# Kernel optimization log

Hardware: AMD Instinct MI355X
Metric: run time of the kernel (lower is better)

The kernel has to match this reference:

```python
import jax, jax.numpy as jnp
import numpy as np

G = 56          # voxel grid resolution per axis
N = 65536
K = 27          # 3x3x3 kernel offsets
C_IN = 128
C_OUT = 128


def _build_rulebook():
    """Submanifold conv rulebook: for each kernel offset, (input_row, output_row) pairs.

    Padded to P=N pairs per offset; invalid pairs use in_idx=0 and out_idx=N
    (a dummy output slot that is dropped), so shapes are static.
    """
    rng = np.random.default_rng(0)
    keys = np.sort(rng.choice(G ** 3, size=N, replace=False)).astype(np.int64)
    x = keys // (G * G)
    y = (keys // G) % G
    z = keys % G
    in_idx = np.zeros((K, N), dtype=np.int32)
    out_idx = np.full((K, N), N, dtype=np.int32)
    k = 0
    for dx in (-1, 0, 1):
        for dy in (-1, 0, 1):
            for dz in (-1, 0, 1):
                nx, ny, nz = x + dx, y + dy, z + dz
                valid = (nx >= 0) & (nx < G) & (ny >= 0) & (ny < G) & (nz >= 0) & (nz < G)
                nkey = (nx * G + ny) * G + nz
                pos = np.searchsorted(keys, np.clip(nkey, 0, G ** 3 - 1))
                pos = np.clip(pos, 0, N - 1)
                found = valid & (keys[pos] == nkey)
                cnt = int(found.sum())
                in_idx[k, :cnt] = pos[found]
                out_idx[k, :cnt] = np.nonzero(found)[0]
                k += 1
    return jnp.asarray(in_idx), jnp.asarray(out_idx)


def setup_inputs() -> dict:
    key = jax.random.key(0)
    k1, k2, k3 = jax.random.split(key, 3)
    fan_in = K * C_IN
    features = jax.random.normal(k1, (N, C_IN), dtype=jnp.float32)
    weight = jax.random.normal(k2, (K, C_IN, C_OUT), dtype=jnp.float32) * (1.0 / np.sqrt(fan_in))
    bias = jax.random.normal(k3, (C_OUT,), dtype=jnp.float32) * 0.01
    in_idx, out_idx = _build_rulebook()
    return {"features": features, "weight": weight, "bias": bias,
            "in_idx": in_idx, "out_idx": out_idx}


def reference(features, weight, bias, in_idx, out_idx):
    # gather: [K, P, C_in]
    gathered = features[in_idx]
    # per-offset GEMM: [K, P, C_out]
    contrib = jnp.einsum('kpc,kcd->kpd', gathered, weight)
    n = features.shape[0]
    c_out = weight.shape[-1]
    # scatter-accumulate into N real rows + 1 dummy row for padded pairs
    out = jnp.zeros((n + 1, c_out), dtype=features.dtype)
    out = out.at[out_idx.reshape(-1)].add(contrib.reshape(-1, c_out))
    return out[:n] + bias
```

## Files before the change

kernel.cpp:

```cpp
#include <hip/hip_runtime.h>
#include <hip/hip_bf16.h>
#include <stdint.h>

#define NV   65536
#define KOFF 27
#define CIN  128
#define COUT 128

typedef __bf16 bf16x8 __attribute__((ext_vector_type(8)));
typedef float  f32x4  __attribute__((ext_vector_type(4)));

__device__ __forceinline__ void async_copy16(void* lds, const void* g) {
    __builtin_amdgcn_global_load_lds(
        (const __attribute__((address_space(1))) void*)g,
        (__attribute__((address_space(3))) void*)lds,
        16, 0, 0);
}

#define JOB_A_BLOCKS 4097
#define JOB_B_BLOCKS 1728
#define JOB_C_BLOCKS 6912

__global__ void k_prep_all(const float* __restrict__ f,
                           uint4* __restrict__ fb4,
                           const float* __restrict__ w,
                           __hip_bfloat16* __restrict__ wt,
                           const int* __restrict__ in_idx,
                           const int* __restrict__ out_idx,
                           int* __restrict__ nbr) {
    const int b = blockIdx.x;
    const int t = threadIdx.x;
    if (b < JOB_A_BLOCKS) {
        int i = b * 256 + t;
        int total8  = (NV + 1) * CIN / 8;
        int nvalid8 = NV * CIN / 8;
        if (i >= total8) return;
        union { uint4 u; __hip_bfloat16 h[8]; } p;
        if (i < nvalid8) {
            const float4* f4 = (const float4*)f;
            float4 a = f4[i * 2];
            float4 c = f4[i * 2 + 1];
            p.h[0] = __float2bfloat16(a.x);
            p.h[1] = __float2bfloat16(a.y);
            p.h[2] = __float2bfloat16(a.z);
            p.h[3] = __float2bfloat16(a.w);
            p.h[4] = __float2bfloat16(c.x);
            p.h[5] = __float2bfloat16(c.y);
            p.h[6] = __float2bfloat16(c.z);
            p.h[7] = __float2bfloat16(c.w);
        } else {
            p.u = make_uint4(0, 0, 0, 0);
        }
        fb4[i] = p.u;
    } else if (b < JOB_A_BLOCKS + JOB_B_BLOCKS) {
        int i = (b - JOB_A_BLOCKS) * 256 + t;
        int k    = i >> 14;
        int cin  = (i >> 7) & 127;
        int cout = i & 127;
        wt[k * 16384 + cout * 128 + cin] = __float2bfloat16(w[i]);
    } else {
        int i = (b - JOB_A_BLOCKS - JOB_B_BLOCKS) * 256 + t;
        int k = i >> 16;
        int p = i & (NV - 1);
        const int* ok = out_idx + k * NV;
        int cur  = ok[p];
        int prev = (p == 0) ? -1 : ok[p - 1];
        int* nb = nbr + k * NV;
        if (cur < NV) nb[cur] = in_idx[k * NV + p];
        for (int j = prev + 1; j < cur && j < NV; ++j) nb[j] = -1;
    }
}

__global__ __launch_bounds__(256, 2)
void sp_conv_main(const __hip_bfloat16* __restrict__ feats,
                  const __hip_bfloat16* __restrict__ wt,
                  const int* __restrict__ nbr,
                  const float* __restrict__ bias,
                  float* __restrict__ out) {
    __shared__ unsigned char smem[65536];
    unsigned char* smA = smem;
    unsigned char* smB = smem + 32768;

    const int t   = threadIdx.x;
    const int bid = blockIdx.x;
    const int tile0 = ((bid & 7) * 64 + (bid >> 3)) * 128;

    const int w    = t >> 6;
    const int lane = t & 63;
    const int lr   = lane & 15;
    const int quad = lane >> 4;
    const int m0   = (w >> 1) * 64;
    const int n0   = (w & 1) * 64;

    const int srow   = t >> 4;
    const int sbyte  = ((t & 15) ^ srow) * 16;

    f32x4 acc[4][4] = {};

    const unsigned char* featsB = (const unsigned char*)feats;
    const unsigned char* wtB    = (const unsigned char*)wt;

    int arows[8];
    {
        const int* nbr0 = nbr + tile0;
        #pragma unroll
        for (int i = 0; i < 8; ++i) arows[i] = nbr0[i * 16 + srow];
    }

    for (int k = 0; k < KOFF; ++k) {
        const unsigned char* wk = wtB + (size_t)k * 32768;
        #pragma unroll
        for (int i = 0; i < 8; ++i) {
            unsigned ar = min((unsigned)arows[i], (unsigned)NV);
            async_copy16(smA + i * 4096 + t * 16,
                         featsB + (size_t)ar * 256 + sbyte);
            async_copy16(smB + i * 4096 + t * 16,
                         wk + (i * 16 + srow) * 256 + sbyte);
        }
        __syncthreads();

        if (k + 1 < KOFF) {
            const int* nbrn = nbr + (k + 1) * NV + tile0;
            #pragma unroll
            for (int i = 0; i < 8; ++i) arows[i] = nbrn[i * 16 + srow];
        }

        #pragma unroll
        for (int ks = 0; ks < 4; ++ks) {
            bf16x8 af[4], bfr[4];
            #pragma unroll
            for (int mt = 0; mt < 4; ++mt) {
                int row = m0 + mt * 16 + lr;
                int pch = ((ks * 4 + quad) ^ lr) * 16;
                af[mt] = *(const bf16x8*)(smA + row * 256 + pch);
            }
            #pragma unroll
            for (int nt = 0; nt < 4; ++nt) {
                int row = n0 + nt * 16 + lr;
                int pch = ((ks * 4 + quad) ^ lr) * 16;
                bfr[nt] = *(const bf16x8*)(smB + row * 256 + pch);
            }
            #pragma unroll
            for (int mt = 0; mt < 4; ++mt)
                #pragma unroll
                for (int nt = 0; nt < 4; ++nt)
                    acc[mt][nt] = __builtin_amdgcn_mfma_f32_16x16x32_bf16(
                        af[mt], bfr[nt], acc[mt][nt], 0, 0, 0);
        }
        __syncthreads();
    }

    float bv[4];
    #pragma unroll
    for (int nt = 0; nt < 4; ++nt) bv[nt] = bias[n0 + nt * 16 + lr];

    #pragma unroll
    for (int mt = 0; mt < 4; ++mt) {
        #pragma unroll
        for (int nt = 0; nt < 4; ++nt) {
            #pragma unroll
            for (int r = 0; r < 4; ++r) {
                int grow = tile0 + m0 + mt * 16 + quad * 4 + r;
                out[(size_t)grow * COUT + n0 + nt * 16 + lr] =
                    acc[mt][nt][r] + bv[nt];
            }
        }
    }
}


extern "C" void kernel_launch(void* const* d_in, const int* in_sizes, int n_in,
                              void* d_out, int out_size, void* d_ws, size_t ws_size,
                              hipStream_t stream) {
    const float* features = (const float*)d_in[0];
    const float* weight   = (const float*)d_in[1];
    const float* bias     = (const float*)d_in[2];
    const int*   in_idx   = (const int*)d_in[3];
    const int*   out_idx  = (const int*)d_in[4];
    float* out = (float*)d_out;

    uint8_t* ws = (uint8_t*)d_ws;
    size_t off = 0;
    __hip_bfloat16* feats_bf = (__hip_bfloat16*)(ws + off);
    off += (size_t)(NV + 1) * CIN * 2;
    off = (off + 255) & ~(size_t)255;
    __hip_bfloat16* wt_bf = (__hip_bfloat16*)(ws + off);
    off += (size_t)KOFF * CIN * COUT * 2;
    off = (off + 255) & ~(size_t)255;
    int* nbr = (int*)(ws + off);

    k_prep_all<<<JOB_A_BLOCKS + JOB_B_BLOCKS + JOB_C_BLOCKS, 256, 0, stream>>>(
        features, (uint4*)feats_bf, weight, wt_bf, in_idx, out_idx, nbr);

    sp_conv_main<<<NV / 128, 256, 0, stream>>>(feats_bf, wt_bf, nbr, bias, out);
}
```

Baseline: 180.2 us.

## Use 32x32 MFMA tiles, LDS-transpose weights, and memset-based neighbor table scatter

The main GEMM loop moves from 16x16x32 MFMA on a 4x4 grid of tiles to 32x32x16 MFMA on a 2x2 grid, which cuts LDS fragment reads per wave and the number of MFMA issues. The weight transpose now stages 64x64 tiles through shared memory so both global reads and writes are coalesced. The neighbor table is built by a memset to -1 followed by a vectorized int4 scatter into an (NV+1)-stride table, so padded pairs land in a dummy slot and the gap-filling loop goes away. This adds an extra memset launch and a larger neighbor table.

```diff
diff --git a/kernel.cpp b/kernel.cpp
--- a/kernel.cpp
+++ b/kernel.cpp
@@ -8,7 +8,7 @@
 #define COUT 128
 
 typedef __bf16 bf16x8 __attribute__((ext_vector_type(8)));
-typedef float  f32x4  __attribute__((ext_vector_type(4)));
+typedef float  f32x16 __attribute__((ext_vector_type(16)));
 
 __device__ __forceinline__ void async_copy16(void* lds, const void* g) {
     __builtin_amdgcn_global_load_lds(
@@ -18,16 +18,17 @@
 }
 
 #define JOB_A_BLOCKS 4097
-#define JOB_B_BLOCKS 1728
-#define JOB_C_BLOCKS 6912
+#define JOB_B_BLOCKS 108
+#define JOB_S_BLOCKS 1728
 
 __global__ void k_prep_all(const float* __restrict__ f,
                            uint4* __restrict__ fb4,
                            const float* __restrict__ w,
                            __hip_bfloat16* __restrict__ wt,
-                           const int* __restrict__ in_idx,
-                           const int* __restrict__ out_idx,
+                           const int4* __restrict__ in4,
+                           const int4* __restrict__ out4,
                            int* __restrict__ nbr) {
+    __shared__ float tb[64][65];
     const int b = blockIdx.x;
     const int t = threadIdx.x;
     if (b < JOB_A_BLOCKS) {
@@ -53,21 +54,35 @@
         }
         fb4[i] = p.u;
     } else if (b < JOB_A_BLOCKS + JOB_B_BLOCKS) {
-        int i = (b - JOB_A_BLOCKS) * 256 + t;
-        int k    = i >> 14;
-        int cin  = (i >> 7) & 127;
-        int cout = i & 127;
-        wt[k * 16384 + cout * 128 + cin] = __float2bfloat16(w[i]);
+        int bb = b - JOB_A_BLOCKS;
+        int k    = bb >> 2;
+        int r0   = ((bb >> 1) & 1) * 64;
+        int c0   = (bb & 1) * 64;
+        const float* wk = w + k * 16384;
+        __hip_bfloat16* wtk = wt + k * 16384;
+        #pragma unroll
+        for (int j = 0; j < 16; ++j) {
+            int lrow = j * 4 + (t >> 6);
+            int lcol = t & 63;
+            tb[lrow][lcol] = wk[(r0 + lrow) * 128 + (c0 + lcol)];
+        }
+        __syncthreads();
+        #pragma unroll
+        for (int j = 0; j < 16; ++j) {
+            int orow = j * 4 + (t >> 6);
+            int ocol = t & 63;
+            wtk[(c0 + orow) * 128 + (r0 + ocol)] = __float2bfloat16(tb[ocol][orow]);
+        }
     } else {
         int i = (b - JOB_A_BLOCKS - JOB_B_BLOCKS) * 256 + t;
-        int k = i >> 16;
-        int p = i & (NV - 1);
-        const int* ok = out_idx + k * NV;
-        int cur  = ok[p];
-        int prev = (p == 0) ? -1 : ok[p - 1];
-        int* nb = nbr + k * NV;
-        if (cur < NV) nb[cur] = in_idx[k * NV + p];
-        for (int j = prev + 1; j < cur && j < NV; ++j) nb[j] = -1;
+        int k = i >> 14;
+        int4 ii = in4[i];
+        int4 oo = out4[i];
+        int* nb = nbr + k * (NV + 1);
+        nb[oo.x] = ii.x;
+        nb[oo.y] = ii.y;
+        nb[oo.z] = ii.z;
+        nb[oo.w] = ii.w;
     }
 }
 
@@ -87,15 +102,15 @@
 
     const int w    = t >> 6;
     const int lane = t & 63;
-    const int lr   = lane & 15;
-    const int quad = lane >> 4;
+    const int l31  = lane & 31;
+    const int half = lane >> 5;
     const int m0   = (w >> 1) * 64;
     const int n0   = (w & 1) * 64;
 
     const int srow   = t >> 4;
     const int sbyte  = ((t & 15) ^ srow) * 16;
 
-    f32x4 acc[4][4] = {};
+    f32x16 acc[2][2] = {};
 
     const unsigned char* featsB = (const unsigned char*)feats;
     const unsigned char* wtB    = (const unsigned char*)wt;
@@ -120,48 +135,48 @@
         __syncthreads();
 
         if (k + 1 < KOFF) {
-            const int* nbrn = nbr + (k + 1) * NV + tile0;
+            const int* nbrn = nbr + (k + 1) * (NV + 1) + tile0;
             #pragma unroll
             for (int i = 0; i < 8; ++i) arows[i] = nbrn[i * 16 + srow];
         }
 
         #pragma unroll
-        for (int ks = 0; ks < 4; ++ks) {
-            bf16x8 af[4], bfr[4];
-            #pragma unroll
-            for (int mt = 0; mt < 4; ++mt) {
-                int row = m0 + mt * 16 + lr;
-                int pch = ((ks * 4 + quad) ^ lr) * 16;
-                af[mt] = *(const bf16x8*)(smA + row * 256 + pch);
+        for (int ks = 0; ks < 8; ++ks) {
+            const int c = ks * 2 + half;
+            bf16x8 af[2], bfr[2];
+            #pragma unroll
+            for (int mt = 0; mt < 2; ++mt) {
+                int row = m0 + mt * 32 + l31;
+                af[mt] = *(const bf16x8*)(smA + row * 256 + ((c ^ (row & 15)) * 16));
             }
             #pragma unroll
-            for (int nt = 0; nt < 4; ++nt) {
-                int row = n0 + nt * 16 + lr;
-                int pch = ((ks * 4 + quad) ^ lr) * 16;
-                bfr[nt] = *(const bf16x8*)(smB + row * 256 + pch);
+            for (int nt = 0; nt < 2; ++nt) {
+                int row = n0 + nt * 32 + l31;
+                bfr[nt] = *(const bf16x8*)(smB + row * 256 + ((c ^ (row & 15)) * 16));
             }
             #pragma unroll
-            for (int mt = 0; mt < 4; ++mt)
+            for (int mt = 0; mt < 2; ++mt)
                 #pragma unroll
-                for (int nt = 0; nt < 4; ++nt)
-                    acc[mt][nt] = __builtin_amdgcn_mfma_f32_16x16x32_bf16(
+                for (int nt = 0; nt < 2; ++nt)
+                    acc[mt][nt] = __builtin_amdgcn_mfma_f32_32x32x16_bf16(
                         af[mt], bfr[nt], acc[mt][nt], 0, 0, 0);
         }
         __syncthreads();
     }
 
-    float bv[4];
+    float bv[2];
     #pragma unroll
-    for (int nt = 0; nt < 4; ++nt) bv[nt] = bias[n0 + nt * 16 + lr];
+    for (int nt = 0; nt < 2; ++nt) bv[nt] = bias[n0 + nt * 32 + l31];
 
     #pragma unroll
-    for (int mt = 0; mt < 4; ++mt) {
-        #pragma unroll
-        for (int nt = 0; nt < 4; ++nt) {
-            #pragma unroll
-            for (int r = 0; r < 4; ++r) {
-                int grow = tile0 + m0 + mt * 16 + quad * 4 + r;
-                out[(size_t)grow * COUT + n0 + nt * 16 + lr] =
+    for (int mt = 0; mt < 2; ++mt) {
+        #pragma unroll
+        for (int nt = 0; nt < 2; ++nt) {
+            #pragma unroll
+            for (int r = 0; r < 16; ++r) {
+                int rrow = (r & 3) + 8 * (r >> 2) + 4 * half;
+                int grow = tile0 + m0 + mt * 32 + rrow;
+                out[(size_t)grow * COUT + n0 + nt * 32 + l31] =
                     acc[mt][nt][r] + bv[nt];
             }
         }
@@ -189,8 +204,11 @@
     off = (off + 255) & ~(size_t)255;
     int* nbr = (int*)(ws + off);
 
-    k_prep_all<<<JOB_A_BLOCKS + JOB_B_BLOCKS + JOB_C_BLOCKS, 256, 0, stream>>>(
-        features, (uint4*)feats_bf, weight, wt_bf, in_idx, out_idx, nbr);
+    hipMemsetAsync(nbr, 0xFF, (size_t)KOFF * (NV + 1) * 4, stream);
+
+    k_prep_all<<<JOB_A_BLOCKS + JOB_B_BLOCKS + JOB_S_BLOCKS, 256, 0, stream>>>(
+        features, (uint4*)feats_bf, weight, wt_bf,
+        (const int4*)in_idx, (const int4*)out_idx, nbr);
 
     sp_conv_main<<<NV / 128, 256, 0, stream>>>(feats_bf, wt_bf, nbr, bias, out);
 }
```

Measured after the change: 167.2 us. 1.08x faster.
